# Performance work log

Measured on AMD Instinct MI355X. Metric: run time of the kernel, lower is better.

Reference implementation:

```python
import jax, jax.numpy as jnp
import numpy as np

EPS = 1e-7          # keras backend epsilon
BN_EPS = 1e-3       # keras BatchNormalization default epsilon
SCALES = (2, 4, 8, 16, 32)  # 2**i for i in 1..max_scale, max_scale=5


def _box_filter(x, k):
    # depthwise conv with all-ones k x k kernel, SAME padding (TF semantics)
    c = x.shape[-1]
    kern = jnp.ones((k, k, 1, c), x.dtype)
    return jax.lax.conv_general_dilated(
        x, kern, (1, 1), 'SAME',
        dimension_numbers=('NHWC', 'HWIO', 'NHWC'),
        feature_group_count=c)


def setup_inputs() -> dict:
    key = jax.random.key(0)
    ks = jax.random.split(key, 4)
    B, H, W, C, R = 16, 56, 56, 128, 8
    x = jax.random.normal(ks[0], (B, H, W, C), jnp.float32)
    kappa = jax.random.uniform(ks[1], (len(SCALES),), jnp.float32, -0.5, 0.5)
    W1 = jax.random.normal(ks[2], (C, C // R), jnp.float32) * (1.0 / np.sqrt(C))
    b1 = jnp.zeros((C // R,), jnp.float32)
    W2 = jax.random.normal(ks[3], (C // R, C), jnp.float32) * (1.0 / np.sqrt(C // R))
    b2 = jnp.zeros((C,), jnp.float32)
    gamma = jnp.ones((C,), jnp.float32)
    beta = jnp.zeros((C,), jnp.float32)
    bn_mean = jnp.zeros((C,), jnp.float32)
    bn_var = jnp.ones((C,), jnp.float32)
    return dict(x=x, kappa=kappa, W1=W1, b1=b1, W2=W2, b2=b2,
                gamma=gamma, beta=beta, bn_mean=bn_mean, bn_var=bn_var)


def reference(x, kappa, W1, b1, W2, b2, gamma, beta, bn_mean, bn_var):
    # per-sample min-max scaling over (H, W, C)
    xmin = jnp.min(x, axis=(1, 2, 3), keepdims=True)
    xmax = jnp.max(x, axis=(1, 2, 3), keepdims=True)
    xs = (x - xmin) / (xmax - xmin + EPS)

    # multi-scale box measures: [B,H,W,C,S]
    measures = jnp.stack([_box_filter(xs, k) for k in SCALES], axis=-1)
    log_m = jnp.log(measures + EPS)
    log_r = jnp.log(jnp.asarray(SCALES, jnp.float32))  # [S]

    # OLS slope of log_m vs log_r along scale axis -> alphas [B,H,W,C]
    xc = log_r - jnp.mean(log_r)
    alphas = jnp.sum(log_m * xc, axis=-1) / jnp.sum(xc * xc)

    # squeeze-and-excite on alphas
    squeeze = jnp.mean(alphas, axis=(1, 2))            # [B,C]
    hidden = jax.nn.relu(squeeze @ W1 + b1)            # [B,C//r]
    excite = jax.nn.sigmoid(hidden @ W2 + b2)          # [B,C]

    # weighted OLS estimate: alpha * (log_k + log_r) -> [B,H,W,C,S]
    k_ = jax.nn.sigmoid(kappa)
    log_k = jax.nn.sigmoid(jnp.log(k_ + EPS))          # [S]
    wols = alphas[..., None] * (log_k + log_r)

    # standardized (mean-centered) cosine similarity along scale axis, in [0,1]
    a = log_m - jnp.mean(log_m, axis=-1, keepdims=True)
    b = wols - jnp.mean(wols, axis=-1, keepdims=True)
    cos = jnp.sum(a * b, axis=-1) / (
        jnp.linalg.norm(a, axis=-1) * jnp.linalg.norm(b, axis=-1) + EPS)
    sim = 0.5 * (cos + 1.0)                            # [B,H,W,C]

    # inference-mode batchnorm on alphas
    alpha_norm = gamma * (alphas - bn_mean) * jax.lax.rsqrt(bn_var + BN_EPS) + beta

    x_exc = xs * excite[:, None, None, :]
    return sim * jax.nn.sigmoid(alpha_norm) + (1.0 - sim) * x_exc
```

## Files before the change

### kernel.cpp

```cpp
#include <hip/hip_runtime.h>
#include <hip/hip_fp16.h>

#define NTOT   6422528
#define NPERB  401408
#define HH     56
#define WW     56
#define CC     128
#define RS     7296
#define SB     415872

__device__ __forceinline__ float sigmoidf_fast(float x) {
    return __builtin_amdgcn_rcpf(1.f + __expf(-x));
}

__device__ __forceinline__ void kappa_consts(const float* kap, float* dcs) {
    float v[5]; float mean = 0.f;
    for (int s = 0; s < 5; s++) {
        float lr = 0.6931471805599453f * (float)(s + 1);
        float k_ = 1.f / (1.f + expf(-kap[s]));
        float lk = 1.f / (1.f + expf(-logf(k_ + 1e-7f)));
        v[s] = lk + lr; mean += v[s];
    }
    mean *= 0.2f; float nd = 0.f;
    for (int s = 0; s < 5; s++) { float d = v[s] - mean; dcs[s] = d; nd += d * d; }
    dcs[5] = sqrtf(nd);
}

__global__ void k_colsum(const float* __restrict__ x, float* __restrict__ S,
                         float* __restrict__ pmn, float* __restrict__ pmx) {
    int t = blockIdx.x * 256 + threadIdx.x;
    int b = t / 7168, r = t % 7168;
    int jm1 = r >> 7, c = r & 127;
    int xbase = b * NPERB + jm1 * 128 + c;
    int scol  = b * SB + (jm1 + 1) * 128 + c;
    S[scol] = 0.f;
    if (jm1 == 0) S[b * SB + c] = 0.f;
    float mn = 3.4e38f, mx = -3.4e38f;
    float acc = 0.f;
    for (int i = 1; i <= HH; i++) {
        float xv = x[xbase + (i - 1) * 7168];
        mn = fminf(mn, xv); mx = fmaxf(mx, xv);
        acc += xv;
        S[scol + i * RS] = acc;
    }
    __shared__ float rmn[256], rmx[256];
    rmn[threadIdx.x] = mn; rmx[threadIdx.x] = mx;
    __syncthreads();
    for (int s = 128; s > 0; s >>= 1) {
        if (threadIdx.x < s) {
            rmn[threadIdx.x] = fminf(rmn[threadIdx.x], rmn[threadIdx.x + s]);
            rmx[threadIdx.x] = fmaxf(rmx[threadIdx.x], rmx[threadIdx.x + s]);
        }
        __syncthreads();
    }
    if (threadIdx.x == 0) { pmn[blockIdx.x] = rmn[0]; pmx[blockIdx.x] = rmx[0]; }
}

__global__ void k_rowsum(float* __restrict__ S, const float* __restrict__ kap,
                         const float* __restrict__ pmn, const float* __restrict__ pmx,
                         float* __restrict__ xmn, float* __restrict__ xiv,
                         float* __restrict__ dcs, float* __restrict__ sq) {
    if (blockIdx.x == 448) {
        int t = threadIdx.x;
        for (int k = t; k < 2048; k += 256) sq[k] = 0.f;
        if (t < 16) {
            float mn = 3.4e38f, mx = -3.4e38f;
            for (int k = 0; k < 28; k++) {
                mn = fminf(mn, pmn[t * 28 + k]);
                mx = fmaxf(mx, pmx[t * 28 + k]);
            }
            xmn[t] = mn;
            xiv[t] = 1.f / (mx - mn + 1e-7f);
        } else if (t == 32) kappa_consts(kap, dcs);
        return;
    }
    int t = blockIdx.x * 256 + threadIdx.x;
    int b = t / 7168, r = t % 7168;
    int i = (r >> 7) + 1, c = r & 127;
    int base = b * SB + i * RS + c;
    S[base] = 0.f;
    float acc = 0.f;
    for (int j = 1; j <= WW; j++) {
        acc += S[base + j * 128];
        S[base + j * 128] = acc;
    }
}

struct ScaleU { int rb1, rb0; float xmch; };

__global__ void k_gather(const float* __restrict__ S, const float* __restrict__ x,
                         const float* __restrict__ gam, const float* __restrict__ bet,
                         const float* __restrict__ bnm, const float* __restrict__ bnv,
                         const float* __restrict__ xmn, const float* __restrict__ xiv,
                         const float* __restrict__ dcs, float* __restrict__ sq,
                         unsigned int* __restrict__ ABu) {
    int p_ = blockIdx.x;
    int L  = (p_ & 7) * 448 + (p_ >> 3);
    int b = L / 224, rem = L % 224;
    int i = rem >> 2, q = rem & 3;
    int c = threadIdx.x & 127, half = threadIdx.x >> 7;
    const float* sp = S + b * SB + c;
    float g = gam[c], be = bet[c], bm = bnm[c];
    float rs = rsqrtf(bnv[c] + 1e-3f);
    float xm = xmn[b], xi = xiv[b];
    float d0 = dcs[0], d1 = dcs[1], d2 = dcs[2], d3 = dcs[3], d4 = dcs[4], nd = dcs[5];

    auto mkU = [&](int hk) {
        ScaleU u;
        int y1g = min(i + hk, HH - 1) + 1;
        int y0g = max(i - hk + 1, 0);
        u.rb1 = y1g * RS; u.rb0 = y0g * RS;
        u.xmch = xm * (float)(y1g - y0g);
        return u;
    };
    ScaleU u0 = mkU(1), u1 = mkU(2), u2 = mkU(4), u3 = mkU(8), u4 = mkU(16);

    auto meas = [&](int j, const ScaleU& u, int hk) -> float {
        int x1g = min(j + hk, WW - 1) + 1;
        int x0g = max(j - hk + 1, 0);
        float cw = (float)(x1g - x0g);
        int o1 = x1g << 7, o0 = x0g << 7;
        float s = sp[u.rb1 + o1] - sp[u.rb0 + o1] - sp[u.rb1 + o0] + sp[u.rb0 + o0];
        return __logf(fmaxf((s - u.xmch * cw) * xi, 0.f) + 1e-7f);
    };

    float asum = 0.f;
    int j0 = q * 14 + half * 7;
    for (int jj = 0; jj < 7; jj++) {
        int j = j0 + jj;
        float l0 = meas(j, u0, 1);
        float l1 = meas(j, u1, 2);
        float l2 = meas(j, u2, 4);
        float l3 = meas(j, u3, 8);
        float l4 = meas(j, u4, 16);
        float w  = -2.f * l0 - l1 + l3 + 2.f * l4;
        asum += w;
        float alphas = w * 0.14426950408889634f;
        float mean = 0.2f * (l0 + l1 + l2 + l3 + l4);
        float a0 = l0 - mean, a1 = l1 - mean, a2 = l2 - mean, a3 = l3 - mean, a4 = l4 - mean;
        float na2  = a0 * a0 + a1 * a1 + a2 * a2 + a3 * a3 + a4 * a4;
        float adot = a0 * d0 + a1 * d1 + a2 * d2 + a3 * d3 + a4 * d4;
        float na = __builtin_amdgcn_sqrtf(na2);
        float cosv = (alphas * adot) * __builtin_amdgcn_rcpf(na * fabsf(alphas) * nd + 1e-7f);
        float sim = 0.5f * (cosv + 1.f);
        float sbn = sigmoidf_fast(g * (alphas - bm) * rs + be);
        int idx = b * NPERB + i * 7168 + j * 128 + c;
        float xs = (x[idx] - xm) * xi;
        float A = sim * sbn;
        float B = (1.f - sim) * xs;
        __half2 h2 = __floats2half2_rn(A, B);
        ABu[idx] = __builtin_bit_cast(unsigned int, h2);
    }
    asum *= 0.14426950408889634f;
    __shared__ float red[256];
    red[threadIdx.x] = asum;
    __syncthreads();
    if (threadIdx.x < 128)
        atomicAdd(&sq[b * 128 + threadIdx.x], red[threadIdx.x] + red[threadIdx.x + 128]);
}

__global__ void k_se(const float* __restrict__ sq, const float* __restrict__ W1,
                     const float* __restrict__ b1, const float* __restrict__ W2,
                     const float* __restrict__ b2, float* __restrict__ exc) {
    __shared__ float sqs[2048];
    __shared__ float hid[256];
    int t = threadIdx.x;
    for (int k = t; k < 2048; k += 256) sqs[k] = sq[k] * (1.f / 3136.f);
    __syncthreads();
    {
        int b = t >> 4, h = t & 15;
        float acc = b1[h];
        for (int c2 = 0; c2 < 128; c2++) acc += sqs[b * 128 + c2] * W1[c2 * 16 + h];
        hid[b * 16 + h] = fmaxf(acc, 0.f);
    }
    __syncthreads();
    for (int k = t; k < 2048; k += 256) {
        int b = k >> 7, c2 = k & 127;
        float acc = b2[c2];
#pragma unroll
        for (int h = 0; h < 16; h++) acc += hid[b * 16 + h] * W2[h * 128 + c2];
        exc[k] = sigmoidf_fast(acc);
    }
}

__global__ void k_mix(const unsigned int* __restrict__ ABu,
                      const float* __restrict__ exc, float* __restrict__ out) {
    int t = blockIdx.x * 256 + threadIdx.x;
    int flat = t * 4;
    int b = flat / NPERB, cb = flat & 127;
    uint4 u = ((const uint4*)ABu)[t];
    float4 e = *(const float4*)(exc + b * 128 + cb);
    float2 p0 = __half22float2(__builtin_bit_cast(__half2, u.x));
    float2 p1 = __half22float2(__builtin_bit_cast(__half2, u.y));
    float2 p2 = __half22float2(__builtin_bit_cast(__half2, u.z));
    float2 p3 = __half22float2(__builtin_bit_cast(__half2, u.w));
    ((float4*)out)[t] = make_float4(p0.x + p0.y * e.x,
                                    p1.x + p1.y * e.y,
                                    p2.x + p2.y * e.z,
                                    p3.x + p3.y * e.w);
}

extern "C" void kernel_launch(void* const* d_in, const int* in_sizes, int n_in,
                              void* d_out, int out_size, void* d_ws, size_t ws_size,
                              hipStream_t stream) {
    const float* x   = (const float*)d_in[0];
    const float* kap = (const float*)d_in[1];
    const float* W1  = (const float*)d_in[2];
    const float* b1  = (const float*)d_in[3];
    const float* W2  = (const float*)d_in[4];
    const float* b2  = (const float*)d_in[5];
    const float* gam = (const float*)d_in[6];
    const float* bet = (const float*)d_in[7];
    const float* bnm = (const float*)d_in[8];
    const float* bnv = (const float*)d_in[9];
    float* out = (float*)d_out;

    float*        S   = (float*)d_ws;
    unsigned int* ABu = (unsigned int*)(S + 16 * SB);
    float* sq  = (float*)(ABu + NTOT);
    float* pmn = sq + 2048;
    float* pmx = pmn + 512;
    float* xmn = pmx + 512;
    float* xiv = xmn + 16;
    float* dcs = xiv + 16;
    float* exc = dcs + 8;

    k_colsum<<<448, 256, 0, stream>>>(x, S, pmn, pmx);
    k_rowsum<<<449, 256, 0, stream>>>(S, kap, pmn, pmx, xmn, xiv, dcs, sq);
    k_gather<<<3584, 256, 0, stream>>>(S, x, gam, bet, bnm, bnv, xmn, xiv, dcs, sq, ABu);
    k_se<<<1, 256, 0, stream>>>(sq, W1, b1, W2, b2, exc);
    k_mix<<<6272, 256, 0, stream>>>(ABu, exc, out);
}
```

Before: 158.8 us.

## Split prefix scans in two segments, use log2 math, fuse SE into mix

The column and row prefix-sum kernels now split each 56-long scan into two 28-element halves run by separate thread groups, joined through shared memory. This doubles the block count and halves the serial dependency chain. The gather kernel switches to log2 with pre-folded batchnorm and sigmoid constants, which removes multiplies. The single-block SE kernel is merged into the mix kernel: every block recomputes the excitation in shared memory, then grid-strides over the output. That saves a launch but repeats the small MLP in each of 1024 blocks.

```diff
diff --git a/kernel.cpp b/kernel.cpp
--- a/kernel.cpp
+++ b/kernel.cpp
@@ -8,6 +8,7 @@
 #define CC     128
 #define RS     7296
 #define SB     415872
+#define LOG2E  1.4426950408889634f
 
 __device__ __forceinline__ float sigmoidf_fast(float x) {
     return __builtin_amdgcn_rcpf(1.f + __expf(-x));
@@ -28,22 +29,43 @@
 
 __global__ void k_colsum(const float* __restrict__ x, float* __restrict__ S,
                          float* __restrict__ pmn, float* __restrict__ pmx) {
-    int t = blockIdx.x * 256 + threadIdx.x;
-    int b = t / 7168, r = t % 7168;
-    int jm1 = r >> 7, c = r & 127;
-    int xbase = b * NPERB + jm1 * 128 + c;
-    int scol  = b * SB + (jm1 + 1) * 128 + c;
-    S[scol] = 0.f;
-    if (jm1 == 0) S[b * SB + c] = 0.f;
+    int p = blockIdx.x;
+    int b = p / 56, j = p % 56;
+    int c = threadIdx.x & 127, seg = threadIdx.x >> 7;
+    int xbase = b * NPERB + j * 128 + c;
+    int scol  = b * SB + (j + 1) * 128 + c;
+    __shared__ float tot[128];
+    __shared__ float rmn[256], rmx[256];
     float mn = 3.4e38f, mx = -3.4e38f;
-    float acc = 0.f;
-    for (int i = 1; i <= HH; i++) {
-        float xv = x[xbase + (i - 1) * 7168];
-        mn = fminf(mn, xv); mx = fmaxf(mx, xv);
-        acc += xv;
-        S[scol + i * RS] = acc;
-    }
-    __shared__ float rmn[256], rmx[256];
+    float v[28];
+    if (seg == 0) {
+        S[scol] = 0.f;
+        if (j == 0) S[b * SB + c] = 0.f;
+        float acc = 0.f;
+#pragma unroll
+        for (int k = 0; k < 28; k++) {
+            float xv = x[xbase + k * 7168];
+            mn = fminf(mn, xv); mx = fmaxf(mx, xv);
+            acc += xv;
+            S[scol + (k + 1) * RS] = acc;
+        }
+        tot[c] = acc;
+    } else {
+        float acc = 0.f;
+#pragma unroll
+        for (int k = 0; k < 28; k++) {
+            float xv = x[xbase + (28 + k) * 7168];
+            mn = fminf(mn, xv); mx = fmaxf(mx, xv);
+            acc += xv;
+            v[k] = acc;
+        }
+    }
+    __syncthreads();
+    if (seg == 1) {
+        float base = tot[c];
+#pragma unroll
+        for (int k = 0; k < 28; k++) S[scol + (29 + k) * RS] = base + v[k];
+    }
     rmn[threadIdx.x] = mn; rmx[threadIdx.x] = mx;
     __syncthreads();
     for (int s = 128; s > 0; s >>= 1) {
@@ -53,36 +75,55 @@
         }
         __syncthreads();
     }
-    if (threadIdx.x == 0) { pmn[blockIdx.x] = rmn[0]; pmx[blockIdx.x] = rmx[0]; }
+    if (threadIdx.x == 0) { pmn[p] = rmn[0]; pmx[p] = rmx[0]; }
 }
 
 __global__ void k_rowsum(float* __restrict__ S, const float* __restrict__ kap,
                          const float* __restrict__ pmn, const float* __restrict__ pmx,
                          float* __restrict__ xmn, float* __restrict__ xiv,
                          float* __restrict__ dcs, float* __restrict__ sq) {
-    if (blockIdx.x == 448) {
+    int p = blockIdx.x;
+    if (p == 896) {
         int t = threadIdx.x;
         for (int k = t; k < 2048; k += 256) sq[k] = 0.f;
         if (t < 16) {
             float mn = 3.4e38f, mx = -3.4e38f;
-            for (int k = 0; k < 28; k++) {
-                mn = fminf(mn, pmn[t * 28 + k]);
-                mx = fmaxf(mx, pmx[t * 28 + k]);
+            for (int k = 0; k < 56; k++) {
+                mn = fminf(mn, pmn[t * 56 + k]);
+                mx = fmaxf(mx, pmx[t * 56 + k]);
             }
             xmn[t] = mn;
             xiv[t] = 1.f / (mx - mn + 1e-7f);
         } else if (t == 32) kappa_consts(kap, dcs);
         return;
     }
-    int t = blockIdx.x * 256 + threadIdx.x;
-    int b = t / 7168, r = t % 7168;
-    int i = (r >> 7) + 1, c = r & 127;
-    int base = b * SB + i * RS + c;
-    S[base] = 0.f;
-    float acc = 0.f;
-    for (int j = 1; j <= WW; j++) {
-        acc += S[base + j * 128];
-        S[base + j * 128] = acc;
+    int b = p / 56, i = (p % 56) + 1;
+    int c = threadIdx.x & 127, seg = threadIdx.x >> 7;
+    int rowbase = b * SB + i * RS + c;
+    __shared__ float tot[128];
+    float v[28];
+    if (seg == 0) {
+        S[rowbase] = 0.f;
+        float acc = 0.f;
+#pragma unroll
+        for (int k = 0; k < 28; k++) {
+            acc += S[rowbase + (k + 1) * 128];
+            S[rowbase + (k + 1) * 128] = acc;
+        }
+        tot[c] = acc;
+    } else {
+        float acc = 0.f;
+#pragma unroll
+        for (int k = 0; k < 28; k++) {
+            acc += S[rowbase + (29 + k) * 128];
+            v[k] = acc;
+        }
+    }
+    __syncthreads();
+    if (seg == 1) {
+        float base = tot[c];
+#pragma unroll
+        for (int k = 0; k < 28; k++) S[rowbase + (29 + k) * 128] = base + v[k];
     }
 }
 
@@ -103,6 +144,10 @@
     float g = gam[c], be = bet[c], bm = bnm[c];
     float rs = rsqrtf(bnv[c] + 1e-3f);
     float xm = xmn[b], xi = xiv[b];
+    float xmxi = xm * xi;
+    float A1 = g * rs, A0 = be - g * bm * rs;
+    float C1 = -A1 * (LOG2E * 0.1f);
+    float C0 = -A0 * LOG2E;
     float d0 = dcs[0], d1 = dcs[1], d2 = dcs[2], d3 = dcs[3], d4 = dcs[4], nd = dcs[5];
 
     auto mkU = [&](int hk) {
@@ -121,7 +166,7 @@
         float cw = (float)(x1g - x0g);
         int o1 = x1g << 7, o0 = x0g << 7;
         float s = sp[u.rb1 + o1] - sp[u.rb0 + o1] - sp[u.rb1 + o0] + sp[u.rb0 + o0];
-        return __logf(fmaxf((s - u.xmch * cw) * xi, 0.f) + 1e-7f);
+        return __log2f(fmaxf((s - u.xmch * cw) * xi, 0.f) + 1e-7f);
     };
 
     float asum = 0.f;
@@ -133,9 +178,9 @@
         float l2 = meas(j, u2, 4);
         float l3 = meas(j, u3, 8);
         float l4 = meas(j, u4, 16);
-        float w  = -2.f * l0 - l1 + l3 + 2.f * l4;
-        asum += w;
-        float alphas = w * 0.14426950408889634f;
+        float w2 = -2.f * l0 - l1 + l3 + 2.f * l4;
+        asum += w2;
+        float alphas = w2 * 0.1f;
         float mean = 0.2f * (l0 + l1 + l2 + l3 + l4);
         float a0 = l0 - mean, a1 = l1 - mean, a2 = l2 - mean, a3 = l3 - mean, a4 = l4 - mean;
         float na2  = a0 * a0 + a1 * a1 + a2 * a2 + a3 * a3 + a4 * a4;
@@ -143,15 +188,15 @@
         float na = __builtin_amdgcn_sqrtf(na2);
         float cosv = (alphas * adot) * __builtin_amdgcn_rcpf(na * fabsf(alphas) * nd + 1e-7f);
         float sim = 0.5f * (cosv + 1.f);
-        float sbn = sigmoidf_fast(g * (alphas - bm) * rs + be);
+        float sbn = __builtin_amdgcn_rcpf(1.f + exp2f(C1 * w2 + C0));
         int idx = b * NPERB + i * 7168 + j * 128 + c;
-        float xs = (x[idx] - xm) * xi;
+        float xs = fmaf(x[idx], xi, -xmxi);
         float A = sim * sbn;
         float B = (1.f - sim) * xs;
         __half2 h2 = __floats2half2_rn(A, B);
         ABu[idx] = __builtin_bit_cast(unsigned int, h2);
     }
-    asum *= 0.14426950408889634f;
+    asum *= 0.1f;
     __shared__ float red[256];
     red[threadIdx.x] = asum;
     __syncthreads();
@@ -159,45 +204,44 @@
         atomicAdd(&sq[b * 128 + threadIdx.x], red[threadIdx.x] + red[threadIdx.x + 128]);
 }
 
-__global__ void k_se(const float* __restrict__ sq, const float* __restrict__ W1,
-                     const float* __restrict__ b1, const float* __restrict__ W2,
-                     const float* __restrict__ b2, float* __restrict__ exc) {
-    __shared__ float sqs[2048];
+__launch_bounds__(256)
+__global__ void k_mix(const unsigned int* __restrict__ ABu, const float* __restrict__ sq,
+                      const float* __restrict__ W1, const float* __restrict__ b1,
+                      const float* __restrict__ W2, const float* __restrict__ b2,
+                      float* __restrict__ out) {
+    __shared__ float buf[2048];
     __shared__ float hid[256];
-    int t = threadIdx.x;
-    for (int k = t; k < 2048; k += 256) sqs[k] = sq[k] * (1.f / 3136.f);
+    int tid = threadIdx.x;
+    for (int k = tid; k < 2048; k += 256) buf[k] = sq[k] * (1.f / 3136.f);
     __syncthreads();
     {
-        int b = t >> 4, h = t & 15;
+        int bb = tid >> 4, h = tid & 15;
         float acc = b1[h];
-        for (int c2 = 0; c2 < 128; c2++) acc += sqs[b * 128 + c2] * W1[c2 * 16 + h];
-        hid[b * 16 + h] = fmaxf(acc, 0.f);
-    }
-    __syncthreads();
-    for (int k = t; k < 2048; k += 256) {
-        int b = k >> 7, c2 = k & 127;
+        for (int c2 = 0; c2 < 128; c2++) acc += buf[bb * 128 + c2] * W1[c2 * 16 + h];
+        hid[bb * 16 + h] = fmaxf(acc, 0.f);
+    }
+    __syncthreads();
+    for (int k = tid; k < 2048; k += 256) {
+        int bb = k >> 7, c2 = k & 127;
         float acc = b2[c2];
 #pragma unroll
-        for (int h = 0; h < 16; h++) acc += hid[b * 16 + h] * W2[h * 128 + c2];
-        exc[k] = sigmoidf_fast(acc);
-    }
-}
-
-__global__ void k_mix(const unsigned int* __restrict__ ABu,
-                      const float* __restrict__ exc, float* __restrict__ out) {
-    int t = blockIdx.x * 256 + threadIdx.x;
-    int flat = t * 4;
-    int b = flat / NPERB, cb = flat & 127;
-    uint4 u = ((const uint4*)ABu)[t];
-    float4 e = *(const float4*)(exc + b * 128 + cb);
-    float2 p0 = __half22float2(__builtin_bit_cast(__half2, u.x));
-    float2 p1 = __half22float2(__builtin_bit_cast(__half2, u.y));
-    float2 p2 = __half22float2(__builtin_bit_cast(__half2, u.z));
-    float2 p3 = __half22float2(__builtin_bit_cast(__half2, u.w));
-    ((float4*)out)[t] = make_float4(p0.x + p0.y * e.x,
-                                    p1.x + p1.y * e.y,
-                                    p2.x + p2.y * e.z,
-                                    p3.x + p3.y * e.w);
+        for (int h = 0; h < 16; h++) acc += hid[bb * 16 + h] * W2[h * 128 + c2];
+        buf[k] = sigmoidf_fast(acc);
+    }
+    __syncthreads();
+    for (int t = blockIdx.x * 256 + tid; t < NTOT / 4; t += 1024 * 256) {
+        int flat = t * 4;
+        int b = flat / NPERB, cb = flat & 127;
+        uint4 u = ((const uint4*)ABu)[t];
+        float2 p0 = __half22float2(__builtin_bit_cast(__half2, u.x));
+        float2 p1 = __half22float2(__builtin_bit_cast(__half2, u.y));
+        float2 p2 = __half22float2(__builtin_bit_cast(__half2, u.z));
+        float2 p3 = __half22float2(__builtin_bit_cast(__half2, u.w));
+        ((float4*)out)[t] = make_float4(p0.x + p0.y * buf[b * 128 + cb],
+                                        p1.x + p1.y * buf[b * 128 + cb + 1],
+                                        p2.x + p2.y * buf[b * 128 + cb + 2],
+                                        p3.x + p3.y * buf[b * 128 + cb + 3]);
+    }
 }
 
 extern "C" void kernel_launch(void* const* d_in, const int* in_sizes, int n_in,
@@ -219,15 +263,13 @@
     unsigned int* ABu = (unsigned int*)(S + 16 * SB);
     float* sq  = (float*)(ABu + NTOT);
     float* pmn = sq + 2048;
-    float* pmx = pmn + 512;
-    float* xmn = pmx + 512;
+    float* pmx = pmn + 1024;
+    float* xmn = pmx + 1024;
     float* xiv = xmn + 16;
     float* dcs = xiv + 16;
-    float* exc = dcs + 8;
-
-    k_colsum<<<448, 256, 0, stream>>>(x, S, pmn, pmx);
-    k_rowsum<<<449, 256, 0, stream>>>(S, kap, pmn, pmx, xmn, xiv, dcs, sq);
+
+    k_colsum<<<896, 256, 0, stream>>>(x, S, pmn, pmx);
+    k_rowsum<<<897, 256, 0, stream>>>(S, kap, pmn, pmx, xmn, xiv, dcs, sq);
     k_gather<<<3584, 256, 0, stream>>>(S, x, gam, bet, bnm, bnv, xmn, xiv, dcs, sq, ABu);
-    k_se<<<1, 256, 0, stream>>>(sq, W1, b1, W2, b2, exc);
-    k_mix<<<6272, 256, 0, stream>>>(ABu, exc, out);
-}
+    k_mix<<<1024, 256, 0, stream>>>(ABu, sq, W1, b1, W2, b2, out);
+}
```

Result: faster. 152.8 us (-3.8%).
